# Kernel tuning notes

Measured on AMD Instinct MI355X. Metric: run time of the kernel, lower is better.

## Reference

```python
import jax, jax.numpy as jnp
import numpy as np

EPS = 1e-08
N_CODECS = 1024

def setup_inputs() -> dict:
    key = jax.random.key(0)
    indices = jax.random.randint(key, (16, 1048576), 0, N_CODECS, dtype=jnp.int64 if jax.config.jax_enable_x64 else jnp.int32)
    return {"indices": indices}

def reference(indices) -> jnp.ndarray:
    # Faithful to: encodings = eq(arange[:,None], flat[None,:]); probs = mean(encodings, dim=1)
    # mean of one-hot over N == count/N, so use a histogram (bincount) instead of the
    # O(n_codecs x N) boolean matrix.
    flat = indices.reshape(-1)
    counts = jnp.bincount(flat, length=N_CODECS)  # [n_codecs]
    probs = counts.astype(jnp.float32) / flat.shape[0]
    perplexity = jnp.exp(-jnp.sum(probs * jnp.log(probs + EPS)))
    return perplexity
```

## Files before the change

### kernel.cpp

```cpp
#include <hip/hip_runtime.h>
#include <hip/hip_bf16.h>

#define N_CODECS 1024
#define EPS 1e-8f
#define HIST_BLOCKS 1024
#define CHUNKS 16

__global__ void __launch_bounds__(256) hist_partial_kernel(
        const int* __restrict__ idx,
        unsigned int* __restrict__ gpart,
        int n4) {
    __shared__ unsigned int lcounts[N_CODECS];
    #pragma unroll
    for (int i = threadIdx.x; i < N_CODECS; i += 256) lcounts[i] = 0u;
    __syncthreads();

    const int4* __restrict__ idx4 = (const int4*)idx;
    const int stride = gridDim.x * 256;
    for (int i = blockIdx.x * 256 + threadIdx.x; i < n4; i += 2 * stride) {
        int4 a = idx4[i];
        int j = i + stride;
        bool has_b = (j < n4);
        int4 b = has_b ? idx4[j] : make_int4(0, 0, 0, 0);

        atomicAdd(&lcounts[a.x], 1u);
        atomicAdd(&lcounts[a.y], 1u);
        atomicAdd(&lcounts[a.z], 1u);
        atomicAdd(&lcounts[a.w], 1u);
        if (has_b) {
            atomicAdd(&lcounts[b.x], 1u);
            atomicAdd(&lcounts[b.y], 1u);
            atomicAdd(&lcounts[b.z], 1u);
            atomicAdd(&lcounts[b.w], 1u);
        }
    }
    __syncthreads();

    unsigned int* __restrict__ mypart = gpart + (size_t)blockIdx.x * N_CODECS;
    #pragma unroll
    for (int i = 0; i < N_CODECS / 256; ++i) {
        int b = i * 256 + threadIdx.x;
        mypart[b] = lcounts[b];
    }
}

__global__ void __launch_bounds__(256) reduce_kernel(
        const unsigned int* __restrict__ gpart,
        unsigned int* __restrict__ p2) {
    int c = blockIdx.x >> 2;
    int q = blockIdx.x & 3;
    int bin = q * 256 + threadIdx.x;

    const unsigned int* __restrict__ base = gpart + (size_t)(c * 64) * N_CODECS + bin;
    unsigned int s0 = 0, s1 = 0, s2 = 0, s3 = 0;
    #pragma unroll 4
    for (int k = 0; k < 64; k += 4) {
        s0 += base[(size_t)(k + 0) * N_CODECS];
        s1 += base[(size_t)(k + 1) * N_CODECS];
        s2 += base[(size_t)(k + 2) * N_CODECS];
        s3 += base[(size_t)(k + 3) * N_CODECS];
    }
    p2[c * N_CODECS + bin] = s0 + s1 + s2 + s3;
}

__global__ void __launch_bounds__(1024) finalize_kernel(
        const unsigned int* __restrict__ p2,
        float* __restrict__ out,
        float invN) {
    int t = threadIdx.x;
    unsigned int cnt = 0;
    #pragma unroll
    for (int c = 0; c < CHUNKS; ++c) cnt += p2[c * N_CODECS + t];

    float p = (float)cnt * invN;
    float term = p * logf(p + EPS);

    #pragma unroll
    for (int off = 32; off > 0; off >>= 1) term += __shfl_down(term, off, 64);

    __shared__ float wsum[16];
    int wave = t >> 6;
    int lane = t & 63;
    if (lane == 0) wsum[wave] = term;
    __syncthreads();

    if (wave == 0) {
        float s = (lane < 16) ? wsum[lane] : 0.0f;
        #pragma unroll
        for (int off = 8; off > 0; off >>= 1) s += __shfl_down(s, off, 64);
        if (lane == 0) out[0] = expf(-s);
    }
}

extern "C" void kernel_launch(void* const* d_in, const int* in_sizes, int n_in,
                              void* d_out, int out_size, void* d_ws, size_t ws_size,
                              hipStream_t stream) {
    const int* indices = (const int*)d_in[0];
    int n = in_sizes[0];
    float* out = (float*)d_out;

    unsigned int* gpart = (unsigned int*)d_ws;
    unsigned int* p2    = gpart + (size_t)HIST_BLOCKS * N_CODECS;

    int n4 = n >> 2;

    hist_partial_kernel<<<HIST_BLOCKS, 256, 0, stream>>>(indices, gpart, n4);
    reduce_kernel<<<CHUNKS * 4, 256, 0, stream>>>(gpart, p2);
    finalize_kernel<<<1, 1024, 0, stream>>>(p2, out, 1.0f / (float)n);
}
```

Baseline: 93.37 us.

## Fuse histogram, reduction and perplexity into one kernel with last-block finalize

Replaces the three-kernel pipeline (per-block partial histograms, chunked reduce, finalize) with a single kernel. Each block atomically merges its shared-memory histogram into one of 8 global copies, and the last block to finish, found via an atomic ticket counter, computes the entropy and exp. It also switches to 256 blocks of 512 threads with 4 int4 loads in flight per iteration. This removes two launches and the 4 MB partial-histogram round trip, at the cost of a memset launch, global atomic contention, and a serialized tail in the last block.

```diff
diff --git a/kernel.cpp b/kernel.cpp
--- a/kernel.cpp
+++ b/kernel.cpp
@@ -3,91 +3,97 @@
 
 #define N_CODECS 1024
 #define EPS 1e-8f
-#define HIST_BLOCKS 1024
-#define CHUNKS 16
+#define BLOCKS 256
+#define THREADS 512
+#define NCOPIES 8
 
-__global__ void __launch_bounds__(256) hist_partial_kernel(
+__global__ void __launch_bounds__(THREADS) fused_hist_perplexity(
         const int* __restrict__ idx,
-        unsigned int* __restrict__ gpart,
-        int n4) {
+        unsigned int* __restrict__ ghist,
+        unsigned int* __restrict__ done,
+        float* __restrict__ out,
+        int n4, float invN) {
     __shared__ unsigned int lcounts[N_CODECS];
     #pragma unroll
-    for (int i = threadIdx.x; i < N_CODECS; i += 256) lcounts[i] = 0u;
+    for (int i = threadIdx.x; i < N_CODECS; i += THREADS) lcounts[i] = 0u;
     __syncthreads();
 
     const int4* __restrict__ idx4 = (const int4*)idx;
-    const int stride = gridDim.x * 256;
-    for (int i = blockIdx.x * 256 + threadIdx.x; i < n4; i += 2 * stride) {
+    const int S = gridDim.x * THREADS;
+    for (int i = blockIdx.x * THREADS + threadIdx.x; i < n4; i += 4 * S) {
+        int i1 = i + S, i2 = i + 2 * S, i3 = i + 3 * S;
+        bool h1 = i1 < n4, h2 = i2 < n4, h3 = i3 < n4;
         int4 a = idx4[i];
-        int j = i + stride;
-        bool has_b = (j < n4);
-        int4 b = has_b ? idx4[j] : make_int4(0, 0, 0, 0);
+        int4 b = h1 ? idx4[i1] : make_int4(0, 0, 0, 0);
+        int4 c = h2 ? idx4[i2] : make_int4(0, 0, 0, 0);
+        int4 d = h3 ? idx4[i3] : make_int4(0, 0, 0, 0);
 
         atomicAdd(&lcounts[a.x], 1u);
         atomicAdd(&lcounts[a.y], 1u);
         atomicAdd(&lcounts[a.z], 1u);
         atomicAdd(&lcounts[a.w], 1u);
-        if (has_b) {
+        if (h1) {
             atomicAdd(&lcounts[b.x], 1u);
             atomicAdd(&lcounts[b.y], 1u);
             atomicAdd(&lcounts[b.z], 1u);
             atomicAdd(&lcounts[b.w], 1u);
         }
+        if (h2) {
+            atomicAdd(&lcounts[c.x], 1u);
+            atomicAdd(&lcounts[c.y], 1u);
+            atomicAdd(&lcounts[c.z], 1u);
+            atomicAdd(&lcounts[c.w], 1u);
+        }
+        if (h3) {
+            atomicAdd(&lcounts[d.x], 1u);
+            atomicAdd(&lcounts[d.y], 1u);
+            atomicAdd(&lcounts[d.z], 1u);
+            atomicAdd(&lcounts[d.w], 1u);
+        }
     }
     __syncthreads();
 
-    unsigned int* __restrict__ mypart = gpart + (size_t)blockIdx.x * N_CODECS;
+    unsigned int* __restrict__ mycopy = ghist + (size_t)(blockIdx.x & (NCOPIES - 1)) * N_CODECS;
     #pragma unroll
-    for (int i = 0; i < N_CODECS / 256; ++i) {
-        int b = i * 256 + threadIdx.x;
-        mypart[b] = lcounts[b];
+    for (int i = threadIdx.x; i < N_CODECS; i += THREADS)
+        atomicAdd(&mycopy[i], lcounts[i]);
+
+    __syncthreads();
+
+    __shared__ unsigned int ticket;
+    if (threadIdx.x == 0) {
+        __threadfence();
+        ticket = atomicAdd(done, 1u);
     }
-}
+    __syncthreads();
+    if (ticket != (unsigned int)(gridDim.x - 1)) return;
 
-__global__ void __launch_bounds__(256) reduce_kernel(
-        const unsigned int* __restrict__ gpart,
-        unsigned int* __restrict__ p2) {
-    int c = blockIdx.x >> 2;
-    int q = blockIdx.x & 3;
-    int bin = q * 256 + threadIdx.x;
-
-    const unsigned int* __restrict__ base = gpart + (size_t)(c * 64) * N_CODECS + bin;
-    unsigned int s0 = 0, s1 = 0, s2 = 0, s3 = 0;
-    #pragma unroll 4
-    for (int k = 0; k < 64; k += 4) {
-        s0 += base[(size_t)(k + 0) * N_CODECS];
-        s1 += base[(size_t)(k + 1) * N_CODECS];
-        s2 += base[(size_t)(k + 2) * N_CODECS];
-        s3 += base[(size_t)(k + 3) * N_CODECS];
+    __threadfence();
+    int t = threadIdx.x;
+    float term = 0.0f;
+    #pragma unroll
+    for (int b = t; b < N_CODECS; b += THREADS) {
+        unsigned int cnt = 0;
+        #pragma unroll
+        for (int cpy = 0; cpy < NCOPIES; ++cpy)
+            cnt += atomicAdd(&ghist[(size_t)cpy * N_CODECS + b], 0u);
+        float p = (float)cnt * invN;
+        term += p * logf(p + EPS);
     }
-    p2[c * N_CODECS + bin] = s0 + s1 + s2 + s3;
-}
-
-__global__ void __launch_bounds__(1024) finalize_kernel(
-        const unsigned int* __restrict__ p2,
-        float* __restrict__ out,
-        float invN) {
-    int t = threadIdx.x;
-    unsigned int cnt = 0;
-    #pragma unroll
-    for (int c = 0; c < CHUNKS; ++c) cnt += p2[c * N_CODECS + t];
-
-    float p = (float)cnt * invN;
-    float term = p * logf(p + EPS);
 
     #pragma unroll
     for (int off = 32; off > 0; off >>= 1) term += __shfl_down(term, off, 64);
 
-    __shared__ float wsum[16];
+    __shared__ float wsum[THREADS / 64];
     int wave = t >> 6;
     int lane = t & 63;
     if (lane == 0) wsum[wave] = term;
     __syncthreads();
 
     if (wave == 0) {
-        float s = (lane < 16) ? wsum[lane] : 0.0f;
+        float s = (lane < THREADS / 64) ? wsum[lane] : 0.0f;
         #pragma unroll
-        for (int off = 8; off > 0; off >>= 1) s += __shfl_down(s, off, 64);
+        for (int off = 4; off > 0; off >>= 1) s += __shfl_down(s, off, 64);
         if (lane == 0) out[0] = expf(-s);
     }
 }
@@ -99,12 +105,13 @@
     int n = in_sizes[0];
     float* out = (float*)d_out;
 
-    unsigned int* gpart = (unsigned int*)d_ws;
-    unsigned int* p2    = gpart + (size_t)HIST_BLOCKS * N_CODECS;
+    unsigned int* ghist = (unsigned int*)d_ws;
+    unsigned int* done  = ghist + (size_t)NCOPIES * N_CODECS;
 
     int n4 = n >> 2;
 
-    hist_partial_kernel<<<HIST_BLOCKS, 256, 0, stream>>>(indices, gpart, n4);
-    reduce_kernel<<<CHUNKS * 4, 256, 0, stream>>>(gpart, p2);
-    finalize_kernel<<<1, 1024, 0, stream>>>(p2, out, 1.0f / (float)n);
+    hipMemsetAsync(d_ws, 0, ((size_t)NCOPIES * N_CODECS + 64) * sizeof(unsigned int), stream);
+
+    fused_hist_perplexity<<<BLOCKS, THREADS, 0, stream>>>(
+        indices, ghist, done, out, n4, 1.0f / (float)n);
 }
```

After: 98.07 us. +5.0%, slower.

## Fuse histogram, reduction and perplexity into one cooperative kernel with grid syncs

Applied to the files above, without the earlier changes.

Replaces the three-kernel pipeline (partial histograms, chunked reduce, finalize) with a single cooperative launch of 256 blocks of 1024 threads. Each block builds a shared-memory histogram, writes it out, then after a grid sync reduces four bins across all block partials and computes their entropy terms, and block 0 combines them after a second grid sync. This removes two kernel launches and the intermediate buffer, and shrinks the number of partial histograms. In exchange it pays for grid-wide barriers, and fewer, larger blocks give less latency hiding and more shared-atomic contention per block.

```diff
diff --git a/kernel.cpp b/kernel.cpp
--- a/kernel.cpp
+++ b/kernel.cpp
@@ -1,25 +1,32 @@
 #include <hip/hip_runtime.h>
-#include <hip/hip_bf16.h>
+#include <hip/hip_cooperative_groups.h>
+
+namespace cg = cooperative_groups;
 
 #define N_CODECS 1024
 #define EPS 1e-8f
-#define HIST_BLOCKS 1024
-#define CHUNKS 16
+#define BLOCKS 256
+#define THREADS 1024
 
-__global__ void __launch_bounds__(256) hist_partial_kernel(
+__global__ void __launch_bounds__(THREADS) fused_hist_perplexity(
         const int* __restrict__ idx,
         unsigned int* __restrict__ gpart,
-        int n4) {
+        float* __restrict__ bterm,
+        float* __restrict__ out,
+        int n4, float invN) {
+    cg::grid_group grid = cg::this_grid();
+
     __shared__ unsigned int lcounts[N_CODECS];
-    #pragma unroll
-    for (int i = threadIdx.x; i < N_CODECS; i += 256) lcounts[i] = 0u;
+    __shared__ float lred[16];
+
+    lcounts[threadIdx.x] = 0u;
     __syncthreads();
 
     const int4* __restrict__ idx4 = (const int4*)idx;
-    const int stride = gridDim.x * 256;
-    for (int i = blockIdx.x * 256 + threadIdx.x; i < n4; i += 2 * stride) {
+    const int S = gridDim.x * THREADS;
+    for (int i = blockIdx.x * THREADS + threadIdx.x; i < n4; i += 2 * S) {
         int4 a = idx4[i];
-        int j = i + stride;
+        int j = i + S;
         bool has_b = (j < n4);
         int4 b = has_b ? idx4[j] : make_int4(0, 0, 0, 0);
 
@@ -36,59 +43,46 @@
     }
     __syncthreads();
 
-    unsigned int* __restrict__ mypart = gpart + (size_t)blockIdx.x * N_CODECS;
-    #pragma unroll
-    for (int i = 0; i < N_CODECS / 256; ++i) {
-        int b = i * 256 + threadIdx.x;
-        mypart[b] = lcounts[b];
-    }
-}
+    gpart[(size_t)blockIdx.x * N_CODECS + threadIdx.x] = lcounts[threadIdx.x];
 
-__global__ void __launch_bounds__(256) reduce_kernel(
-        const unsigned int* __restrict__ gpart,
-        unsigned int* __restrict__ p2) {
-    int c = blockIdx.x >> 2;
-    int q = blockIdx.x & 3;
-    int bin = q * 256 + threadIdx.x;
+    grid.sync();
 
-    const unsigned int* __restrict__ base = gpart + (size_t)(c * 64) * N_CODECS + bin;
-    unsigned int s0 = 0, s1 = 0, s2 = 0, s3 = 0;
-    #pragma unroll 4
-    for (int k = 0; k < 64; k += 4) {
-        s0 += base[(size_t)(k + 0) * N_CODECS];
-        s1 += base[(size_t)(k + 1) * N_CODECS];
-        s2 += base[(size_t)(k + 2) * N_CODECS];
-        s3 += base[(size_t)(k + 3) * N_CODECS];
-    }
-    p2[c * N_CODECS + bin] = s0 + s1 + s2 + s3;
-}
-
-__global__ void __launch_bounds__(1024) finalize_kernel(
-        const unsigned int* __restrict__ p2,
-        float* __restrict__ out,
-        float invN) {
     int t = threadIdx.x;
-    unsigned int cnt = 0;
-    #pragma unroll
-    for (int c = 0; c < CHUNKS; ++c) cnt += p2[c * N_CODECS + t];
-
-    float p = (float)cnt * invN;
-    float term = p * logf(p + EPS);
+    int bin = 4 * blockIdx.x + (t >> 8);
+    int row = t & 255;
+    unsigned int v = gpart[(size_t)row * N_CODECS + bin];
 
     #pragma unroll
-    for (int off = 32; off > 0; off >>= 1) term += __shfl_down(term, off, 64);
+    for (int off = 32; off > 0; off >>= 1) v += __shfl_down(v, off, 64);
 
-    __shared__ float wsum[16];
-    int wave = t >> 6;
-    int lane = t & 63;
-    if (lane == 0) wsum[wave] = term;
+    int wave = t >> 6, lane = t & 63;
+    if (lane == 0) lred[wave] = (float)v;
     __syncthreads();
 
-    if (wave == 0) {
-        float s = (lane < 16) ? wsum[lane] : 0.0f;
+    if (t < 4) {
+        float cnt = lred[4 * t] + lred[4 * t + 1] + lred[4 * t + 2] + lred[4 * t + 3];
+        float p = cnt * invN;
+        float term = p * logf(p + EPS);
+        term += __shfl_down(term, 2, 64);
+        term += __shfl_down(term, 1, 64);
+        if (t == 0) bterm[blockIdx.x] = term;
+    }
+
+    grid.sync();
+
+    if (blockIdx.x == 0) {
+        float s = (t < BLOCKS) ? bterm[t] : 0.0f;
         #pragma unroll
-        for (int off = 8; off > 0; off >>= 1) s += __shfl_down(s, off, 64);
-        if (lane == 0) out[0] = expf(-s);
+        for (int off = 32; off > 0; off >>= 1) s += __shfl_down(s, off, 64);
+        __syncthreads();
+        if (lane == 0) lred[wave] = s;
+        __syncthreads();
+        if (t == 0) {
+            float tot = 0.0f;
+            #pragma unroll
+            for (int w = 0; w < 16; ++w) tot += lred[w];
+            out[0] = expf(-tot);
+        }
     }
 }
 
@@ -100,11 +94,13 @@
     float* out = (float*)d_out;
 
     unsigned int* gpart = (unsigned int*)d_ws;
-    unsigned int* p2    = gpart + (size_t)HIST_BLOCKS * N_CODECS;
+    float* bterm = (float*)(gpart + (size_t)BLOCKS * N_CODECS);
 
     int n4 = n >> 2;
+    float invN = 1.0f / (float)n;
 
-    hist_partial_kernel<<<HIST_BLOCKS, 256, 0, stream>>>(indices, gpart, n4);
-    reduce_kernel<<<CHUNKS * 4, 256, 0, stream>>>(gpart, p2);
-    finalize_kernel<<<1, 1024, 0, stream>>>(p2, out, 1.0f / (float)n);
+    void* args[] = { (void*)&indices, (void*)&gpart, (void*)&bterm,
+                     (void*)&out, (void*)&n4, (void*)&invN };
+    hipLaunchCooperativeKernel((const void*)fused_hist_perplexity,
+                               dim3(BLOCKS), dim3(THREADS), args, 0, stream);
 }
```

Measured after the change: 159.9 us. 71.3% more time.

## Fuse reduce and finalize kernels using atomics and a last-block ticket

Applied to the files above, without the earlier changes.

Merges the two-stage partial-histogram reduction and the single-block finalize into one kernel. 128 blocks each sum 8 partial histograms and atomically add the result into a global count array, and the last block to finish (found with a ticket counter) computes the entropy and perplexity. The global counters are zeroed by block 0 of the histogram kernel. This removes one kernel launch and an intermediate buffer round trip, at the cost of global atomics and a threadfence-based completion protocol.

```diff
diff --git a/kernel.cpp b/kernel.cpp
--- a/kernel.cpp
+++ b/kernel.cpp
@@ -1,18 +1,27 @@
 #include <hip/hip_runtime.h>
-#include <hip/hip_bf16.h>
 
 #define N_CODECS 1024
 #define EPS 1e-8f
 #define HIST_BLOCKS 1024
-#define CHUNKS 16
+#define RED_BLOCKS 128
+#define RED_THREADS 512
+#define ROWS_PER_RED (HIST_BLOCKS / RED_BLOCKS)
 
 __global__ void __launch_bounds__(256) hist_partial_kernel(
         const int* __restrict__ idx,
         unsigned int* __restrict__ gpart,
+        unsigned int* __restrict__ cnt,
+        unsigned int* __restrict__ done,
         int n4) {
     __shared__ unsigned int lcounts[N_CODECS];
     #pragma unroll
     for (int i = threadIdx.x; i < N_CODECS; i += 256) lcounts[i] = 0u;
+
+    if (blockIdx.x == 0) {
+        #pragma unroll
+        for (int i = threadIdx.x; i < N_CODECS; i += 256) cnt[i] = 0u;
+        if (threadIdx.x == 0) done[0] = 0u;
+    }
     __syncthreads();
 
     const int4* __restrict__ idx4 = (const int4*)idx;
@@ -44,51 +53,56 @@
     }
 }
 
-__global__ void __launch_bounds__(256) reduce_kernel(
+__global__ void __launch_bounds__(RED_THREADS) reduce_finalize_kernel(
         const unsigned int* __restrict__ gpart,
-        unsigned int* __restrict__ p2) {
-    int c = blockIdx.x >> 2;
-    int q = blockIdx.x & 3;
-    int bin = q * 256 + threadIdx.x;
-
-    const unsigned int* __restrict__ base = gpart + (size_t)(c * 64) * N_CODECS + bin;
-    unsigned int s0 = 0, s1 = 0, s2 = 0, s3 = 0;
-    #pragma unroll 4
-    for (int k = 0; k < 64; k += 4) {
-        s0 += base[(size_t)(k + 0) * N_CODECS];
-        s1 += base[(size_t)(k + 1) * N_CODECS];
-        s2 += base[(size_t)(k + 2) * N_CODECS];
-        s3 += base[(size_t)(k + 3) * N_CODECS];
-    }
-    p2[c * N_CODECS + bin] = s0 + s1 + s2 + s3;
-}
-
-__global__ void __launch_bounds__(1024) finalize_kernel(
-        const unsigned int* __restrict__ p2,
+        unsigned int* __restrict__ cnt,
+        unsigned int* __restrict__ done,
         float* __restrict__ out,
         float invN) {
     int t = threadIdx.x;
-    unsigned int cnt = 0;
+
+    const unsigned int* __restrict__ base =
+        gpart + (size_t)(blockIdx.x * ROWS_PER_RED) * N_CODECS;
+    unsigned int s0 = 0, s1 = 0;
     #pragma unroll
-    for (int c = 0; c < CHUNKS; ++c) cnt += p2[c * N_CODECS + t];
+    for (int r = 0; r < ROWS_PER_RED; ++r) {
+        s0 += base[(size_t)r * N_CODECS + t];
+        s1 += base[(size_t)r * N_CODECS + t + RED_THREADS];
+    }
+    atomicAdd(&cnt[t], s0);
+    atomicAdd(&cnt[t + RED_THREADS], s1);
 
-    float p = (float)cnt * invN;
-    float term = p * logf(p + EPS);
+    __syncthreads();
+
+    __shared__ unsigned int ticket;
+    if (t == 0) {
+        __threadfence();
+        ticket = atomicAdd(done, 1u);
+    }
+    __syncthreads();
+    if (ticket != (unsigned int)(RED_BLOCKS - 1)) return;
+
+    __threadfence();
+    unsigned int c0 = atomicAdd(&cnt[t], 0u);
+    unsigned int c1 = atomicAdd(&cnt[t + RED_THREADS], 0u);
+    float p0 = (float)c0 * invN;
+    float p1 = (float)c1 * invN;
+    float term = p0 * logf(p0 + EPS) + p1 * logf(p1 + EPS);
 
     #pragma unroll
     for (int off = 32; off > 0; off >>= 1) term += __shfl_down(term, off, 64);
 
-    __shared__ float wsum[16];
+    __shared__ float wsum[RED_THREADS / 64];
     int wave = t >> 6;
     int lane = t & 63;
     if (lane == 0) wsum[wave] = term;
     __syncthreads();
 
-    if (wave == 0) {
-        float s = (lane < 16) ? wsum[lane] : 0.0f;
+    if (t == 0) {
+        float s = 0.0f;
         #pragma unroll
-        for (int off = 8; off > 0; off >>= 1) s += __shfl_down(s, off, 64);
-        if (lane == 0) out[0] = expf(-s);
+        for (int w = 0; w < RED_THREADS / 64; ++w) s += wsum[w];
+        out[0] = expf(-s);
     }
 }
 
@@ -100,11 +114,12 @@
     float* out = (float*)d_out;
 
     unsigned int* gpart = (unsigned int*)d_ws;
-    unsigned int* p2    = gpart + (size_t)HIST_BLOCKS * N_CODECS;
+    unsigned int* cnt   = gpart + (size_t)HIST_BLOCKS * N_CODECS;
+    unsigned int* done  = cnt + N_CODECS;
 
     int n4 = n >> 2;
 
-    hist_partial_kernel<<<HIST_BLOCKS, 256, 0, stream>>>(indices, gpart, n4);
-    reduce_kernel<<<CHUNKS * 4, 256, 0, stream>>>(gpart, p2);
-    finalize_kernel<<<1, 1024, 0, stream>>>(p2, out, 1.0f / (float)n);
+    hist_partial_kernel<<<HIST_BLOCKS, 256, 0, stream>>>(indices, gpart, cnt, done, n4);
+    reduce_finalize_kernel<<<RED_BLOCKS, RED_THREADS, 0, stream>>>(
+        gpart, cnt, done, out, 1.0f / (float)n);
 }
```

Measured after the change: 94.91 us. No clear change (+1.6%).
